# Kernel optimization log

Hardware: AMD Instinct MI355X
Metric: run time of the kernel (lower is better)

The kernel has to match this reference:

```python
import jax, jax.numpy as jnp
import numpy as np

DIM = 256
NUM_LAYERS = 64


def setup_inputs() -> dict:
    key = jax.random.key(0)
    kx, kt = jax.random.split(key)
    x = jax.random.normal(kx, (32768, DIM), dtype=jnp.float32)
    # theta[l, p]: scalar angle for pair p in layer l. Odd-offset layers use only
    # the first DIM//2 - 1 entries. Matches torch.randn(()) * pi init.
    theta = jax.random.normal(kt, (NUM_LAYERS, DIM // 2), dtype=jnp.float32) * jnp.pi
    return {"x": x, "theta": theta}


def _apply_layer(x, th, offset):
    """Apply one layer of 2x2 Givens-like rotations to pairs (i, i+1).

    U = [[c, s], [s, -c]] with c=cos(2*theta), s=sin(2*theta); U is symmetric so
    out = vec @ U.T = vec @ U -> yi = c*xi + s*xj, yj = s*xi - c*xj.
    """
    b, d = x.shape
    if offset == 0:
        npairs = d // 2
        c = jnp.cos(2.0 * th[:npairs])  # [npairs]
        s = jnp.sin(2.0 * th[:npairs])
        v = x.reshape(b, npairs, 2)
        xi, xj = v[..., 0], v[..., 1]
        yi = c * xi + s * xj
        yj = s * xi - c * xj
        return jnp.stack([yi, yj], axis=-1).reshape(b, d)
    else:
        npairs = d // 2 - 1
        c = jnp.cos(2.0 * th[:npairs])
        s = jnp.sin(2.0 * th[:npairs])
        inner = x[:, 1:d - 1].reshape(b, npairs, 2)
        xi, xj = inner[..., 0], inner[..., 1]
        yi = c * xi + s * xj
        yj = s * xi - c * xj
        mid = jnp.stack([yi, yj], axis=-1).reshape(b, d - 2)
        return jnp.concatenate([x[:, :1], mid, x[:, d - 1:]], axis=1)


def reference(x, theta):
    # Python loop over num_layers (fixed, small structural set).
    for depth in range(NUM_LAYERS):
        x = _apply_layer(x, theta[depth], depth % 2)
    return x
```

## Files before the change

kernel.cpp:

```cpp
#include <hip/hip_runtime.h>
#include <math.h>

#define DIM 256
#define NLAYERS 64

typedef __attribute__((ext_vector_type(8))) short short8;
typedef __attribute__((ext_vector_type(4))) float f32x4;

__device__ __forceinline__ float dpp_shl1_zero(float v) {
    int r = __builtin_amdgcn_update_dpp(0, __float_as_int(v), 0x130, 0xF, 0xF, true);
    return __int_as_float(r);
}
__device__ __forceinline__ float dpp_shr1_keep(float oldv, float v) {
    int r = __builtin_amdgcn_update_dpp(__float_as_int(oldv), __float_as_int(v), 0x138, 0xF, 0xF, false);
    return __int_as_float(r);
}
__device__ __forceinline__ unsigned short f2bf(float f) {
    unsigned u = __float_as_uint(f);
    u += 0x7FFFu + ((u >> 16) & 1u);
    return (unsigned short)(u >> 16);
}
__device__ __forceinline__ unsigned cvtpk_bf16(float a, float b) {
    unsigned r;
    asm("v_cvt_pk_bf16_f32 %0, %1, %2" : "=v"(r) : "v"(a), "v"(b));
    return r;
}

__global__ __launch_bounds__(1024)
void build_m_kernel(const float* __restrict__ theta, unsigned short* __restrict__ bfrag) {
    __shared__ float tbl[NLAYERS * DIM];
    const int tid = threadIdx.x;
    #pragma unroll
    for (int kk = 0; kk < 8; ++kk) {
        int idx = tid + 1024 * kk;
        int l = idx >> 7, p = idx & 127;
        float a = 2.0f * theta[idx];
        float s = __sinf(a), c = __cosf(a);
        if ((l & 1) && (p == 127)) { c = 1.0f; s = 0.0f; }
        tbl[idx * 2 + 0] = c;
        tbl[idx * 2 + 1] = s;
    }
    __syncthreads();

    const int w = tid >> 6;
    const int t = tid & 63;
    const int row = blockIdx.x * 16 + w;

    float e[4];
    #pragma unroll
    for (int j = 0; j < 4; ++j) e[j] = (4 * t + j == row) ? 1.0f : 0.0f;

    const float4* tbl4 = (const float4*)tbl;
    #pragma unroll 2
    for (int l = 0; l < NLAYERS; l += 2) {
        float4 cs = tbl4[(l << 6) + t];
        {
            float a0 = e[0], a1 = e[1], a2 = e[2], a3 = e[3];
            e[0] = cs.x * a0 + cs.y * a1;
            e[1] = cs.y * a0 - cs.x * a1;
            e[2] = cs.z * a2 + cs.w * a3;
            e[3] = cs.w * a2 - cs.z * a3;
        }
        float4 cs1 = tbl4[((l + 1) << 6) + t];
        {
            float a1 = e[1], a2 = e[2], a3 = e[3];
            float n1 = cs1.x * a1 + cs1.y * a2;
            float n2 = cs1.y * a1 - cs1.x * a2;
            float xjn = dpp_shl1_zero(e[0]);
            float n3  = cs1.z * a3 + cs1.w * xjn;
            float snd = cs1.w * a3 - cs1.z * xjn;
            e[0] = dpp_shr1_keep(e[0], snd);
            e[1] = n1; e[2] = n2; e[3] = n3;
        }
    }

    const int kt = row >> 5, g8 = (row >> 3) & 3, ki = row & 7;
    #pragma unroll
    for (int j = 0; j < 4; ++j) {
        int col = 4 * t + j;
        bfrag[(((col >> 4) * 8 + kt) * 64 + g8 * 16 + (col & 15)) * 8 + ki] = f2bf(e[j]);
    }
}

__global__ __launch_bounds__(512, 4)
void clements_gemm(const float* __restrict__ x,
                   const unsigned short* __restrict__ bfrag,
                   float* __restrict__ out) {
    __shared__ unsigned short abf[4][4096];

    const int tid = threadIdx.x;
    const int w   = tid >> 6;
    const int t   = tid & 63;
    const int l16 = t & 15;
    const int g   = t >> 4;
    const long rowbase = (long)blockIdx.x * 64;

    const int sr = tid >> 5;
    const int so = tid & 31;
    char* const wbase = (char*)&abf[0][0] +
        ((((so >> 2) * 1024) + ((so & 3) * 256) + (sr * 16)) ^ ((so & 7) << 4));
    const float* const xp = x + (rowbase + sr) * 256 + so * 8;

    f32x4 pa[4], pb[4];
#define LOADR(i) { pa[i] = *(const f32x4*)(xp + (i) * 16 * 256);       \
                   pb[i] = *(const f32x4*)(xp + (i) * 16 * 256 + 4); }
#define CVTW(i) { union { short8 s; unsigned u[4]; } h;                \
        h.u[0] = cvtpk_bf16(pa[i][0], pa[i][1]);                       \
        h.u[1] = cvtpk_bf16(pa[i][2], pa[i][3]);                       \
        h.u[2] = cvtpk_bf16(pb[i][0], pb[i][1]);                       \
        h.u[3] = cvtpk_bf16(pb[i][2], pb[i][3]);                       \
        *(short8*)(wbase + (i) * 8192) = h.s; }
#define BAR() { asm volatile("s_waitcnt lgkmcnt(0)" ::: "memory");     \
                __builtin_amdgcn_s_barrier();                          \
                __builtin_amdgcn_sched_barrier(0); }

    short8 Bf[8][2];
    {
        const short8* bp = (const short8*)bfrag;
        #pragma unroll
        for (int nt = 0; nt < 2; ++nt)
            #pragma unroll
            for (int kt = 0; kt < 8; ++kt)
                Bf[kt][nt] = bp[((w * 2 + nt) * 8 + kt) * 64 + t];
    }

    LOADR(0) LOADR(1) LOADR(2)
    CVTW(0)
    BAR()

    const char* const rbase = (const char*)&abf[0][0];
    auto compute = [&](int i) {
        f32x4 a0 = {0.f,0.f,0.f,0.f}, a1 = {0.f,0.f,0.f,0.f};
        #pragma unroll
        for (int kt = 0; kt < 8; ++kt) {
            short8 A = *(const short8*)(rbase + (i) * 8192 +
                ((kt * 1024 + t * 16) ^ (((kt * 4 + g) & 7) << 4)));
            a0 = __builtin_amdgcn_mfma_f32_16x16x32_bf16(A, Bf[kt][0], a0, 0, 0, 0);
            a1 = __builtin_amdgcn_mfma_f32_16x16x32_bf16(A, Bf[kt][1], a1, 0, 0, 0);
        }
        float* o = out + (rowbase + i * 16 + g * 4) * 256 + 32 * w + l16;
        #pragma unroll
        for (int j = 0; j < 4; ++j) {
            o[(long)j * 256 +  0] = a0[j];
            o[(long)j * 256 + 16] = a1[j];
        }
    };

    LOADR(3)
    compute(0);
    CVTW(1)
    BAR()
    compute(1);
    CVTW(2)
    BAR()
    compute(2);
    CVTW(3)
    BAR()
    compute(3);
#undef LOADR
#undef CVTW
#undef BAR
}

__global__ __launch_bounds__(1024, 4)
void clements_direct(const float* __restrict__ x,
                     const float* __restrict__ theta,
                     float* __restrict__ out) {
    __shared__ float tbl[NLAYERS * DIM];
    const int tid = threadIdx.x;
    #pragma unroll
    for (int k = 0; k < 8; ++k) {
        int idx = tid + 1024 * k;
        int l = idx >> 7;
        int p = idx & 127;
        float s, c;
        sincosf(2.0f * theta[idx], &s, &c);
        if ((l & 1) && (p == 127)) { c = 1.0f; s = 0.0f; }
        tbl[idx * 2 + 0] = c;
        tbl[idx * 2 + 1] = s;
    }
    __syncthreads();
    const int w = tid >> 6;
    const int t = tid & 63;
    const long base = ((long)blockIdx.x * 16 + w) * 8;
    float e[8][4];
    #pragma unroll
    for (int r = 0; r < 8; ++r) {
        float4 v = ((const float4*)(x + (base + r) * (long)DIM))[t];
        e[r][0] = v.x; e[r][1] = v.y; e[r][2] = v.z; e[r][3] = v.w;
    }
    const float4* tbl4 = (const float4*)tbl;
    #pragma unroll 2
    for (int l = 0; l < NLAYERS; l += 2) {
        float4 cs = tbl4[(l << 6) + t];
        #pragma unroll
        for (int r = 0; r < 8; ++r) {
            float a0 = e[r][0], a1 = e[r][1], a2 = e[r][2], a3 = e[r][3];
            e[r][0] = cs.x * a0 + cs.y * a1;
            e[r][1] = cs.y * a0 - cs.x * a1;
            e[r][2] = cs.z * a2 + cs.w * a3;
            e[r][3] = cs.w * a2 - cs.z * a3;
        }
        float4 cs1 = tbl4[((l + 1) << 6) + t];
        #pragma unroll
        for (int r = 0; r < 8; ++r) {
            float a1 = e[r][1], a2 = e[r][2], a3 = e[r][3];
            float n1 = cs1.x * a1 + cs1.y * a2;
            float n2 = cs1.y * a1 - cs1.x * a2;
            float xjn = dpp_shl1_zero(e[r][0]);
            float n3  = cs1.z * a3 + cs1.w * xjn;
            float snd = cs1.w * a3 - cs1.z * xjn;
            e[r][0] = dpp_shr1_keep(e[r][0], snd);
            e[r][1] = n1; e[r][2] = n2; e[r][3] = n3;
        }
    }
    #pragma unroll
    for (int r = 0; r < 8; ++r) {
        float4 v;
        v.x = e[r][0]; v.y = e[r][1]; v.z = e[r][2]; v.w = e[r][3];
        ((float4*)(out + (base + r) * (long)DIM))[t] = v;
    }
}

extern "C" void kernel_launch(void* const* d_in, const int* in_sizes, int n_in,
                              void* d_out, int out_size, void* d_ws, size_t ws_size,
                              hipStream_t stream) {
    const float* x     = (const float*)d_in[0];
    const float* theta = (const float*)d_in[1];
    float* out = (float*)d_out;

    const size_t need = (size_t)DIM * DIM * sizeof(unsigned short);
    if (ws_size >= need) {
        unsigned short* bfrag = (unsigned short*)d_ws;
        hipLaunchKernelGGL(build_m_kernel, dim3(16),  dim3(1024), 0, stream, theta, bfrag);
        hipLaunchKernelGGL(clements_gemm,  dim3(512), dim3(512),  0, stream, x, bfrag, out);
    } else {
        hipLaunchKernelGGL(clements_direct, dim3(256), dim3(1024), 0, stream, x, theta, out);
    }
}
```

Before: 25.67 us.

## Double-buffer LDS and process 128 rows per block in a pipelined loop

The GEMM kernel now gives each block 128 rows in eight 16-row chunks instead of 64 rows in four. A two-slot LDS ring buffer and a software-pipelined loop handle the chunks, prefetching the global loads two chunks ahead. The grid drops from 512 to 256 blocks, which halves the redundant per-block loads of the 128KB B fragment set and cuts LDS use per block. The cost is fewer blocks, roughly one per CU, leaving less wave-level parallelism to hide memory latency.

```diff
diff --git a/kernel.cpp b/kernel.cpp
--- a/kernel.cpp
+++ b/kernel.cpp
@@ -86,32 +86,31 @@
 void clements_gemm(const float* __restrict__ x,
                    const unsigned short* __restrict__ bfrag,
                    float* __restrict__ out) {
-    __shared__ unsigned short abf[4][4096];
+    __shared__ unsigned short abf[2][4096];
 
     const int tid = threadIdx.x;
     const int w   = tid >> 6;
     const int t   = tid & 63;
     const int l16 = t & 15;
     const int g   = t >> 4;
-    const long rowbase = (long)blockIdx.x * 64;
+    const long rowbase = (long)blockIdx.x * 128;
 
     const int sr = tid >> 5;
     const int so = tid & 31;
-    char* const wbase = (char*)&abf[0][0] +
-        ((((so >> 2) * 1024) + ((so & 3) * 256) + (sr * 16)) ^ ((so & 7) << 4));
+    const int wsw = (((so >> 2) * 1024) + ((so & 3) * 256) + (sr * 16)) ^ ((so & 7) << 4);
     const float* const xp = x + (rowbase + sr) * 256 + so * 8;
 
-    f32x4 pa[4], pb[4];
-#define LOADR(i) { pa[i] = *(const f32x4*)(xp + (i) * 16 * 256);       \
-                   pb[i] = *(const f32x4*)(xp + (i) * 16 * 256 + 4); }
-#define CVTW(i) { union { short8 s; unsigned u[4]; } h;                \
-        h.u[0] = cvtpk_bf16(pa[i][0], pa[i][1]);                       \
-        h.u[1] = cvtpk_bf16(pa[i][2], pa[i][3]);                       \
-        h.u[2] = cvtpk_bf16(pb[i][0], pb[i][1]);                       \
-        h.u[3] = cvtpk_bf16(pb[i][2], pb[i][3]);                       \
-        *(short8*)(wbase + (i) * 8192) = h.s; }
-#define BAR() { asm volatile("s_waitcnt lgkmcnt(0)" ::: "memory");     \
-                __builtin_amdgcn_s_barrier();                          \
+    f32x4 pa[2], pb[2];
+#define LOADR(i) { pa[(i) & 1] = *(const f32x4*)(xp + (i) * 16 * 256);       \
+                   pb[(i) & 1] = *(const f32x4*)(xp + (i) * 16 * 256 + 4); }
+#define CVTW(i) { union { short8 s; unsigned u[4]; } h;                      \
+        h.u[0] = cvtpk_bf16(pa[(i) & 1][0], pa[(i) & 1][1]);                 \
+        h.u[1] = cvtpk_bf16(pa[(i) & 1][2], pa[(i) & 1][3]);                 \
+        h.u[2] = cvtpk_bf16(pb[(i) & 1][0], pb[(i) & 1][1]);                 \
+        h.u[3] = cvtpk_bf16(pb[(i) & 1][2], pb[(i) & 1][3]);                 \
+        *(short8*)((char*)&abf[(i) & 1][0] + wsw) = h.s; }
+#define BAR() { asm volatile("s_waitcnt lgkmcnt(0)" ::: "memory");           \
+                __builtin_amdgcn_s_barrier();                                \
                 __builtin_amdgcn_sched_barrier(0); }
 
     short8 Bf[8][2];
@@ -124,16 +123,12 @@
                 Bf[kt][nt] = bp[((w * 2 + nt) * 8 + kt) * 64 + t];
     }
 
-    LOADR(0) LOADR(1) LOADR(2)
-    CVTW(0)
-    BAR()
-
-    const char* const rbase = (const char*)&abf[0][0];
     auto compute = [&](int i) {
         f32x4 a0 = {0.f,0.f,0.f,0.f}, a1 = {0.f,0.f,0.f,0.f};
+        const char* rb = (const char*)&abf[i & 1][0];
         #pragma unroll
         for (int kt = 0; kt < 8; ++kt) {
-            short8 A = *(const short8*)(rbase + (i) * 8192 +
+            short8 A = *(const short8*)(rb +
                 ((kt * 1024 + t * 16) ^ (((kt * 4 + g) & 7) << 4)));
             a0 = __builtin_amdgcn_mfma_f32_16x16x32_bf16(A, Bf[kt][0], a0, 0, 0, 0);
             a1 = __builtin_amdgcn_mfma_f32_16x16x32_bf16(A, Bf[kt][1], a1, 0, 0, 0);
@@ -146,17 +141,19 @@
         }
     };
 
-    LOADR(3)
-    compute(0);
-    CVTW(1)
+    LOADR(0) LOADR(1)
+    CVTW(0)
     BAR()
-    compute(1);
-    CVTW(2)
-    BAR()
-    compute(2);
-    CVTW(3)
-    BAR()
-    compute(3);
+
+    #pragma unroll
+    for (int c = 0; c < 8; ++c) {
+        if (c + 2 < 8) LOADR(c + 2)
+        compute(c);
+        if (c + 1 < 8) {
+            CVTW(c + 1)
+            BAR()
+        }
+    }
 #undef LOADR
 #undef CVTW
 #undef BAR
@@ -233,7 +230,7 @@
     if (ws_size >= need) {
         unsigned short* bfrag = (unsigned short*)d_ws;
         hipLaunchKernelGGL(build_m_kernel, dim3(16),  dim3(1024), 0, stream, theta, bfrag);
-        hipLaunchKernelGGL(clements_gemm,  dim3(512), dim3(512),  0, stream, x, bfrag, out);
+        hipLaunchKernelGGL(clements_gemm,  dim3(256), dim3(512),  0, stream, x, bfrag, out);
     } else {
         hipLaunchKernelGGL(clements_direct, dim3(256), dim3(1024), 0, stream, x, theta, out);
     }
```

Result: no change. 25.24 us (-1.7%).
